# Kernel tuning notes

Hardware: AMD Instinct MI355X
Metric: run time of the kernel (lower is better)

Reference implementation:

```python
import jax
import jax.numpy as jnp
from jax import lax
import numpy as np

B, C, H, W = 16, 96, 112, 112
HIDDEN = 4 * C
LN_EPS = 1e-6  # ConvNeXt LayerNorm eps


def setup_inputs() -> dict:
    key = jax.random.key(0)
    ks = jax.random.split(key, 8)
    x = jax.random.normal(ks[0], (B, C, H, W), dtype=jnp.float32)
    # depthwise 7x7 kernel, HWIO with feature_group_count=C -> (7,7,1,C)
    dw_w = jax.random.normal(ks[1], (7, 7, 1, C), dtype=jnp.float32) * 0.02
    dw_b = jnp.zeros((C,), dtype=jnp.float32)
    gamma = jnp.ones((C,), dtype=jnp.float32)
    beta = jnp.zeros((C,), dtype=jnp.float32)
    w1 = jax.random.normal(ks[2], (C, HIDDEN), dtype=jnp.float32) * 0.02
    b1 = jnp.zeros((HIDDEN,), dtype=jnp.float32)
    w2 = jax.random.normal(ks[3], (HIDDEN, C), dtype=jnp.float32) * 0.02
    b2 = jnp.zeros((C,), dtype=jnp.float32)
    scale = jnp.full((C,), 1e-6, dtype=jnp.float32)  # block_scale init 1e-6
    return {"x": x, "dw_w": dw_w, "dw_b": dw_b, "gamma": gamma, "beta": beta,
            "w1": w1, "b1": b1, "w2": w2, "b2": b2, "scale": scale}


def reference(x, dw_w, dw_b, gamma, beta, w1, b1, w2, b2, scale):
    # depthwise 7x7, stride 1, padding 3 (SAME), groups = C
    y = lax.conv_general_dilated(
        x, dw_w, window_strides=(1, 1), padding="SAME",
        dimension_numbers=("NCHW", "HWIO", "NCHW"),
        feature_group_count=C,
    ) + dw_b[None, :, None, None]
    # BCHW -> BHWC
    y = jnp.transpose(y, (0, 2, 3, 1))
    # LayerNorm over channel dim
    mu = jnp.mean(y, axis=-1, keepdims=True)
    var = jnp.var(y, axis=-1, keepdims=True)
    y = (y - mu) * lax.rsqrt(var + LN_EPS) * gamma + beta
    # pointwise MLP with exact GELU (torch nn.GELU default)
    h = jax.nn.gelu(jnp.einsum("bhwc,cd->bhwd", y, w1) + b1, approximate=False)
    y = jnp.einsum("bhwd,dc->bhwc", h, w2) + b2
    # BHWC -> BCHW, scale, residual (eval mode: stochastic depth = identity)
    y = jnp.transpose(y, (0, 3, 1, 2))
    return scale[None, :, None, None] * y + x
```

## Files before the change

### kernel.cpp

```cpp
#include <hip/hip_runtime.h>
#include <hip/hip_bf16.h>

#define BATCH 16
#define CCH 96
#define HH 112
#define WW 112
#define HID 384
#define NPIX (BATCH * HH * WW)
#define HW (HH * WW)

#define PXB 128
#define ZROWD 50
#define SLICE_B 12288
#define RING_SLOTS 3
#define ZR_BYTES (PXB * ZROWD * 4)
#define B1_OFF (RING_SLOTS * SLICE_B)
#define SMEM_TOTAL (B1_OFF + 1536)

#define XSTR 132
#define CXROWS 62

typedef __attribute__((ext_vector_type(8))) short bf16x8;
typedef __attribute__((ext_vector_type(4))) float f32x4;
typedef __attribute__((ext_vector_type(4))) unsigned int uint4v;

typedef const __attribute__((address_space(1))) void gvoid_t;
typedef __attribute__((address_space(3))) void svoid_t;

__device__ __forceinline__ short f2bf(float v) {
    __hip_bfloat16 h = __float2bfloat16(v);
    return __builtin_bit_cast(short, h);
}
__device__ __forceinline__ float bf2f(short s) {
    unsigned int u = ((unsigned int)(unsigned short)s) << 16;
    return __builtin_bit_cast(float, u);
}
__device__ __forceinline__ float gelu_fast(float v) {
    float e = __expf(-1.702f * v);
    return v * __builtin_amdgcn_rcpf(1.0f + e);
}

__global__ __launch_bounds__(256) void pack_w(const float* __restrict__ w1,
                                              const float* __restrict__ w2,
                                              const float* __restrict__ gamma,
                                              const float* __restrict__ scale,
                                              short* __restrict__ wp) {
    int o = blockIdx.x * 256 + threadIdx.x;
    if (o >= 12 * 12 * 64 * 8) return;
    const int j   = o & 7;
    const int l   = (o >> 3) & 63;
    const int g   = o >> 9;
    const int f   = g % 12;
    const int kk2 = g / 12;
    float v;
    if (f < 6) {
        const int kk = f >> 1, mh = f & 1;
        const int c  = kk * 32 + (l >> 4) * 8 + j;
        const int d  = (2 * kk2 + mh) * 16 + (l & 15);
        v = gamma[c] * w1[c * HID + d];
    } else {
        const int nt2 = f - 6;
        const int dd  = kk2 * 32 + ((j >> 2) << 4) + ((l >> 4) << 2) + (j & 3);
        const int n   = nt2 * 16 + (l & 15);
        v = w2[dd * CCH + n] * scale[n];
    }
    wp[o] = f2bf(v);
}

__global__ __launch_bounds__(256) void pack_bias(const float* __restrict__ w1,
                                                 const float* __restrict__ b1,
                                                 const float* __restrict__ beta,
                                                 const float* __restrict__ b2,
                                                 const float* __restrict__ scale,
                                                 float* __restrict__ b1p,
                                                 float* __restrict__ b2p) {
    int t = blockIdx.x * 256 + threadIdx.x;
    if (t < HID) {
        float s = b1[t];
        for (int c = 0; c < CCH; ++c) s += beta[c] * w1[c * HID + t];
        b1p[t] = s;
    } else if (t < HID + CCH) {
        int c = t - HID;
        b2p[c] = scale[c] * b2[c];
    }
}

__global__ __launch_bounds__(256) void conv_kernel(
    const float* __restrict__ x, const float* __restrict__ dww,
    const float* __restrict__ dwb, short* __restrict__ y)
{
    __shared__ float xs[CXROWS * XSTR];

    const int t = threadIdx.x;
    const int p = blockIdx.x;
    int o = (p & 7) * 384 + (p >> 3);
    const int hh = o & 1;  o >>= 1;
    const int c  = o % CCH;
    const int b  = o / CCH;
    const int h0 = hh * 56;
    const float* xc = x + (size_t)(b * CCH + c) * HW;

    float4 vbuf[8];
    #pragma unroll
    for (int k = 0; k < 8; ++k) {
        const int idx = t + 256 * k;
        const int r  = idx >> 5;
        const int j  = idx & 31;
        const int gh = h0 - 3 + r;
        float4 v = make_float4(0.f, 0.f, 0.f, 0.f);
        if (idx < CXROWS * 32 && (unsigned)gh < HH && j >= 1 && j <= 28)
            v = *reinterpret_cast<const float4*>(xc + gh * WW + 4 * j - 4);
        vbuf[k] = v;
    }
    #pragma unroll
    for (int k = 0; k < 8; ++k) {
        const int idx = t + 256 * k;
        if (idx < CXROWS * 32)
            *reinterpret_cast<float4*>(&xs[(idx >> 5) * XSTR + (idx & 31) * 4]) = vbuf[k];
    }
    __syncthreads();

    const int cg = t >> 5;
    const int rg = t & 31;
    if (cg < 7 && rg < 28) {
        const int r0 = rg * 2;
        const int j0 = cg * 16;
        const float bias = dwb[c];
        float acc0[16], acc1[16];
        #pragma unroll
        for (int i = 0; i < 16; ++i) { acc0[i] = bias; acc1[i] = bias; }
        #pragma unroll
        for (int ir = 0; ir < 8; ++ir) {
            f32x4 qd[6];
            #pragma unroll
            for (int u = 0; u < 6; ++u)
                qd[u] = *reinterpret_cast<const f32x4*>(&xs[(r0 + ir) * XSTR + j0 + 4 * u]);
            #pragma unroll
            for (int kw = 0; kw < 7; ++kw) {
                if (ir <= 6) {
                    const float wt = dww[(ir * 7 + kw) * CCH + c];
                    #pragma unroll
                    for (int i = 0; i < 16; ++i) {
                        const int jj = i + kw + 1;
                        acc0[i] += qd[jj >> 2][jj & 3] * wt;
                    }
                }
                if (ir >= 1) {
                    const float wt = dww[((ir - 1) * 7 + kw) * CCH + c];
                    #pragma unroll
                    for (int i = 0; i < 16; ++i) {
                        const int jj = i + kw + 1;
                        acc1[i] += qd[jj >> 2][jj & 3] * wt;
                    }
                }
            }
        }
        uint4v wa, wb2, wc, wd;
        #pragma unroll
        for (int u = 0; u < 4; ++u) {
            wa[u] = (unsigned int)(unsigned short)f2bf(acc0[2 * u]) |
                    ((unsigned int)(unsigned short)f2bf(acc0[2 * u + 1]) << 16);
            wb2[u] = (unsigned int)(unsigned short)f2bf(acc0[8 + 2 * u]) |
                    ((unsigned int)(unsigned short)f2bf(acc0[9 + 2 * u]) << 16);
            wc[u] = (unsigned int)(unsigned short)f2bf(acc1[2 * u]) |
                    ((unsigned int)(unsigned short)f2bf(acc1[2 * u + 1]) << 16);
            wd[u] = (unsigned int)(unsigned short)f2bf(acc1[8 + 2 * u]) |
                    ((unsigned int)(unsigned short)f2bf(acc1[9 + 2 * u]) << 16);
        }
        short* yc = y + (size_t)(b * CCH + c) * HW + (h0 + r0) * WW + j0;
        *reinterpret_cast<uint4v*>(yc)          = wa;
        *reinterpret_cast<uint4v*>(yc + 8)      = wb2;
        *reinterpret_cast<uint4v*>(yc + WW)     = wc;
        *reinterpret_cast<uint4v*>(yc + WW + 8) = wd;
    }
}

__global__ __launch_bounds__(256, 4) void mlp_kernel(
    const short* __restrict__ ybuf, const char* __restrict__ wp,
    const float* __restrict__ b1p, const float* __restrict__ b2p,
    const float* __restrict__ x, float* __restrict__ out)
{
    __shared__ __align__(16) char smem[SMEM_TOTAL];
    unsigned int* zr = (unsigned int*)smem;
    float* b1l = (float*)(smem + B1_OFF);

    const int t    = threadIdx.x;
    const int lane = t & 63;
    const int wv   = t >> 6;
    const int l15  = lane & 15;
    const int q    = lane >> 4;
    const int px0  = blockIdx.x * PXB;
    const int b    = px0 / HW;
    const int hw0  = px0 - b * HW;

    if (t < 192) {
        const int pq = t / 48;
        const int cp = t - pq * 48;
        const unsigned int* Ap = (const unsigned int*)(ybuf +
            (size_t)(b * CCH + 2 * cp) * HW + hw0 + pq * 32);
        const unsigned int* Bp = (const unsigned int*)(ybuf +
            (size_t)(b * CCH + 2 * cp + 1) * HW + hw0 + pq * 32);
        #pragma unroll
        for (int e = 0; e < 4; ++e) {
            const uint4v A  = *reinterpret_cast<const uint4v*>(Ap + e * 4);
            const uint4v Bv = *reinterpret_cast<const uint4v*>(Bp + e * 4);
            #pragma unroll
            for (int k = 0; k < 4; ++k) {
                const int px = pq * 32 + e * 8 + 2 * k;
                zr[px * ZROWD + cp]       = (A[k] & 0xffffu) | (Bv[k] << 16);
                zr[(px + 1) * ZROWD + cp] = (A[k] >> 16) | (Bv[k] & 0xffff0000u);
            }
        }
    } else {
        const int i0 = (t - 192) * 6;
        #pragma unroll
        for (int i2 = 0; i2 < 6; ++i2) b1l[i0 + i2] = b1p[i0 + i2];
    }

    f32x4 acc2[2][6];
    #pragma unroll
    for (int nt2 = 0; nt2 < 6; ++nt2) {
        const int c = nt2 * 16 + l15;
        const float bv = b2p[c];
        #pragma unroll
        for (int m2 = 0; m2 < 2; ++m2) {
            const size_t g = (size_t)(b * CCH + c) * HW + hw0 + wv * 32 + m2 * 16 + q * 4;
            const f32x4 xv = *reinterpret_cast<const f32x4*>(x + g);
            acc2[m2][nt2].x = bv + xv.x;  acc2[m2][nt2].y = bv + xv.y;
            acc2[m2][nt2].z = bv + xv.z;  acc2[m2][nt2].w = bv + xv.w;
        }
    }
    __syncthreads();

    bf16x8 za[2][3];
    #pragma unroll
    for (int nt = 0; nt < 2; ++nt) {
        const int row = wv * 32 + nt * 16 + l15;
        const char* base = smem + row * (ZROWD * 4) + q * 16;
        float s1 = 0.f, s2 = 0.f;
        #pragma unroll
        for (int kk = 0; kk < 3; ++kk) {
            za[nt][kk] = *reinterpret_cast<const bf16x8*>(base + kk * 64);
            #pragma unroll
            for (int j = 0; j < 8; ++j) {
                const float v = bf2f(za[nt][kk][j]);
                s1 += v; s2 += v * v;
            }
        }
        s1 += __shfl_xor(s1, 16, 64);  s2 += __shfl_xor(s2, 16, 64);
        s1 += __shfl_xor(s1, 32, 64);  s2 += __shfl_xor(s2, 32, 64);
        const float mu   = s1 * (1.0f / CCH);
        const float rstd = rsqrtf(s2 * (1.0f / CCH) - mu * mu + 1e-6f);
        #pragma unroll
        for (int kk = 0; kk < 3; ++kk)
            #pragma unroll
            for (int j = 0; j < 8; ++j)
                za[nt][kk][j] = f2bf((bf2f(za[nt][kk][j]) - mu) * rstd);
    }
    __syncthreads();

    asm volatile("s_waitcnt vmcnt(0)" ::: "memory");

    #define STAGE_F(SL, SLOT)                                                       \
        {                                                                           \
            const char* _s = wp + (size_t)(SL) * SLICE_B + (wv * 3) * 1024 +        \
                             lane * 16;                                             \
            char* _d = smem + (SLOT) * SLICE_B + (wv * 3) * 1024;                   \
            __builtin_amdgcn_global_load_lds((gvoid_t*)(_s),        (svoid_t*)(_d),        16, 0, 0); \
            __builtin_amdgcn_global_load_lds((gvoid_t*)(_s + 1024), (svoid_t*)(_d + 1024), 16, 0, 0); \
            __builtin_amdgcn_global_load_lds((gvoid_t*)(_s + 2048), (svoid_t*)(_d + 2048), 16, 0, 0); \
        }
    #define WAITBAR()                                                               \
        {                                                                           \
            asm volatile("s_waitcnt vmcnt(3)" ::: "memory");                        \
            __builtin_amdgcn_s_barrier();                                           \
            __builtin_amdgcn_sched_barrier(0);                                      \
        }

    STAGE_F(0, 0);

    #pragma unroll
    for (int kk2 = 0; kk2 < 12; ++kk2) {
        {
            const int sl = (kk2 + 1 > 11) ? 11 : kk2 + 1;
            STAGE_F(sl, sl % RING_SLOTS);
        }
        WAITBAR();
        const char* wb = smem + (kk2 % RING_SLOTS) * SLICE_B + lane * 16;

        f32x4 p0[2], p1[2];
        const f32x4 bva = *reinterpret_cast<const f32x4*>(b1l + 32 * kk2 + q * 4);
        const f32x4 bvb = *reinterpret_cast<const f32x4*>(b1l + 32 * kk2 + 16 + q * 4);
        p0[0] = bva;  p0[1] = bva;
        p1[0] = bvb;  p1[1] = bvb;
        #pragma unroll
        for (int kk = 0; kk < 3; ++kk) {
            const bf16x8 wfa = *reinterpret_cast<const bf16x8*>(wb + (kk * 2) * 1024);
            const bf16x8 wfb = *reinterpret_cast<const bf16x8*>(wb + (kk * 2 + 1) * 1024);
            p0[0] = __builtin_amdgcn_mfma_f32_16x16x32_bf16(wfa, za[0][kk], p0[0], 0, 0, 0);
            p0[1] = __builtin_amdgcn_mfma_f32_16x16x32_bf16(wfa, za[1][kk], p0[1], 0, 0, 0);
            p1[0] = __builtin_amdgcn_mfma_f32_16x16x32_bf16(wfb, za[0][kk], p1[0], 0, 0, 0);
            p1[1] = __builtin_amdgcn_mfma_f32_16x16x32_bf16(wfb, za[1][kk], p1[1], 0, 0, 0);
        }
        bf16x8 hv[2];
        #pragma unroll
        for (int nt = 0; nt < 2; ++nt)
            #pragma unroll
            for (int i = 0; i < 4; ++i) {
                hv[nt][i]     = f2bf(gelu_fast(p0[nt][i]));
                hv[nt][4 + i] = f2bf(gelu_fast(p1[nt][i]));
            }
        #pragma unroll
        for (int nt2 = 0; nt2 < 6; ++nt2) {
            const bf16x8 bfr = *reinterpret_cast<const bf16x8*>(wb + (6 + nt2) * 1024);
            acc2[0][nt2] = __builtin_amdgcn_mfma_f32_16x16x32_bf16(hv[0], bfr, acc2[0][nt2], 0, 0, 0);
            acc2[1][nt2] = __builtin_amdgcn_mfma_f32_16x16x32_bf16(hv[1], bfr, acc2[1][nt2], 0, 0, 0);
        }
    }
    #undef STAGE_F
    #undef WAITBAR

    #pragma unroll
    for (int m2 = 0; m2 < 2; ++m2) {
        const int pxl = hw0 + wv * 32 + m2 * 16 + q * 4;
        #pragma unroll
        for (int nt2 = 0; nt2 < 6; ++nt2) {
            const int c = nt2 * 16 + l15;
            const size_t g = (size_t)(b * CCH + c) * HW + pxl;
            *reinterpret_cast<f32x4*>(out + g) = acc2[m2][nt2];
        }
    }
}

extern "C" void kernel_launch(void* const* d_in, const int* in_sizes, int n_in,
                              void* d_out, int out_size, void* d_ws, size_t ws_size,
                              hipStream_t stream) {
    const float* x     = (const float*)d_in[0];
    const float* dww   = (const float*)d_in[1];
    const float* dwb   = (const float*)d_in[2];
    const float* gamma = (const float*)d_in[3];
    const float* beta  = (const float*)d_in[4];
    const float* w1    = (const float*)d_in[5];
    const float* b1    = (const float*)d_in[6];
    const float* w2    = (const float*)d_in[7];
    const float* b2    = (const float*)d_in[8];
    const float* scale = (const float*)d_in[9];
    float* out = (float*)d_out;

    char* ws = (char*)d_ws;
    short* ybuf = (short*)ws;
    const size_t Y_BYTES = (size_t)NPIX * CCH * 2;
    short* wp  = (short*)(ws + Y_BYTES);
    float* b1p = (float*)(ws + Y_BYTES + 12 * SLICE_B);
    float* b2p = b1p + HID;

    pack_w<<<(12 * 12 * 64 * 8 + 255) / 256, 256, 0, stream>>>(w1, w2, gamma, scale, wp);
    pack_bias<<<2, 256, 0, stream>>>(w1, b1, beta, b2, scale, b1p, b2p);
    conv_kernel<<<BATCH * CCH * 2, 256, 0, stream>>>(x, dww, dwb, ybuf);
    mlp_kernel<<<NPIX / PXB, 256, 0, stream>>>(ybuf, (const char*)wp, b1p, b2p, x, out);
}
```

Baseline: 112.4 us.

## Split MLP tile across eight waves with sixteen pixels per wave

The MLP kernel now launches 512 threads per block instead of 256, so each of the eight waves owns 16 pixels rather than 32. Per-wave accumulators and normalized activations shrink, cutting register use so more waves can be resident and hide memory latency. Weight staging into LDS is spread across six waves with two loads each, and the bias preload and transpose are reassigned to the larger thread count. In exchange, each weight fragment read from LDS now feeds half as many MFMAs, doubling LDS read traffic per FLOP and adding more barrier participants.

Result: slower. 135.4 us (+20.5%).

```diff
diff --git a/kernel.cpp b/kernel.cpp
--- a/kernel.cpp
+++ b/kernel.cpp
@@ -175,7 +175,7 @@
     }
 }
 
-__global__ __launch_bounds__(256, 4) void mlp_kernel(
+__global__ __launch_bounds__(512, 8) void mlp_kernel(
     const short* __restrict__ ybuf, const char* __restrict__ wp,
     const float* __restrict__ b1p, const float* __restrict__ b2p,
     const float* __restrict__ x, float* __restrict__ out)
@@ -193,57 +193,53 @@
     const int b    = px0 / HW;
     const int hw0  = px0 - b * HW;
 
-    if (t < 192) {
-        const int pq = t / 48;
-        const int cp = t - pq * 48;
+    if (t < 384) {
+        const int pxq = t / 48;
+        const int cp  = t - pxq * 48;
         const unsigned int* Ap = (const unsigned int*)(ybuf +
-            (size_t)(b * CCH + 2 * cp) * HW + hw0 + pq * 32);
+            (size_t)(b * CCH + 2 * cp) * HW + hw0 + pxq * 16);
         const unsigned int* Bp = (const unsigned int*)(ybuf +
-            (size_t)(b * CCH + 2 * cp + 1) * HW + hw0 + pq * 32);
-        #pragma unroll
-        for (int e = 0; e < 4; ++e) {
+            (size_t)(b * CCH + 2 * cp + 1) * HW + hw0 + pxq * 16);
+        #pragma unroll
+        for (int e = 0; e < 2; ++e) {
             const uint4v A  = *reinterpret_cast<const uint4v*>(Ap + e * 4);
             const uint4v Bv = *reinterpret_cast<const uint4v*>(Bp + e * 4);
             #pragma unroll
             for (int k = 0; k < 4; ++k) {
-                const int px = pq * 32 + e * 8 + 2 * k;
+                const int px = pxq * 16 + e * 8 + 2 * k;
                 zr[px * ZROWD + cp]       = (A[k] & 0xffffu) | (Bv[k] << 16);
                 zr[(px + 1) * ZROWD + cp] = (A[k] >> 16) | (Bv[k] & 0xffff0000u);
             }
         }
     } else {
-        const int i0 = (t - 192) * 6;
-        #pragma unroll
-        for (int i2 = 0; i2 < 6; ++i2) b1l[i0 + i2] = b1p[i0 + i2];
-    }
-
-    f32x4 acc2[2][6];
+        const int i0 = (t - 384) * 3;
+        #pragma unroll
+        for (int i2 = 0; i2 < 3; ++i2) b1l[i0 + i2] = b1p[i0 + i2];
+    }
+
+    f32x4 acc2[6];
     #pragma unroll
     for (int nt2 = 0; nt2 < 6; ++nt2) {
         const int c = nt2 * 16 + l15;
         const float bv = b2p[c];
-        #pragma unroll
-        for (int m2 = 0; m2 < 2; ++m2) {
-            const size_t g = (size_t)(b * CCH + c) * HW + hw0 + wv * 32 + m2 * 16 + q * 4;
-            const f32x4 xv = *reinterpret_cast<const f32x4*>(x + g);
-            acc2[m2][nt2].x = bv + xv.x;  acc2[m2][nt2].y = bv + xv.y;
-            acc2[m2][nt2].z = bv + xv.z;  acc2[m2][nt2].w = bv + xv.w;
-        }
+        const size_t g = (size_t)(b * CCH + c) * HW + hw0 + wv * 16 + q * 4;
+        const f32x4 xv = *reinterpret_cast<const f32x4*>(x + g);
+        acc2[nt2].x = bv + xv.x;  acc2[nt2].y = bv + xv.y;
+        acc2[nt2].z = bv + xv.z;  acc2[nt2].w = bv + xv.w;
     }
     __syncthreads();
 
-    bf16x8 za[2][3];
-    #pragma unroll
-    for (int nt = 0; nt < 2; ++nt) {
-        const int row = wv * 32 + nt * 16 + l15;
+    bf16x8 za[3];
+    {
+        const int row = wv * 16 + l15;
         const char* base = smem + row * (ZROWD * 4) + q * 16;
         float s1 = 0.f, s2 = 0.f;
         #pragma unroll
         for (int kk = 0; kk < 3; ++kk) {
-            za[nt][kk] = *reinterpret_cast<const bf16x8*>(base + kk * 64);
+            za[kk] = *reinterpret_cast<const bf16x8*>(base + kk * 64);
             #pragma unroll
             for (int j = 0; j < 8; ++j) {
-                const float v = bf2f(za[nt][kk][j]);
+                const float v = bf2f(za[kk][j]);
                 s1 += v; s2 += v * v;
             }
         }
@@ -255,24 +251,23 @@
         for (int kk = 0; kk < 3; ++kk)
             #pragma unroll
             for (int j = 0; j < 8; ++j)
-                za[nt][kk][j] = f2bf((bf2f(za[nt][kk][j]) - mu) * rstd);
+                za[kk][j] = f2bf((bf2f(za[kk][j]) - mu) * rstd);
     }
     __syncthreads();
 
     asm volatile("s_waitcnt vmcnt(0)" ::: "memory");
 
     #define STAGE_F(SL, SLOT)                                                       \
-        {                                                                           \
-            const char* _s = wp + (size_t)(SL) * SLICE_B + (wv * 3) * 1024 +        \
+        if (wv < 6) {                                                               \
+            const char* _s = wp + (size_t)(SL) * SLICE_B + (wv * 2) * 1024 +        \
                              lane * 16;                                             \
-            char* _d = smem + (SLOT) * SLICE_B + (wv * 3) * 1024;                   \
+            char* _d = smem + (SLOT) * SLICE_B + (wv * 2) * 1024;                   \
             __builtin_amdgcn_global_load_lds((gvoid_t*)(_s),        (svoid_t*)(_d),        16, 0, 0); \
             __builtin_amdgcn_global_load_lds((gvoid_t*)(_s + 1024), (svoid_t*)(_d + 1024), 16, 0, 0); \
-            __builtin_amdgcn_global_load_lds((gvoid_t*)(_s + 2048), (svoid_t*)(_d + 2048), 16, 0, 0); \
         }
     #define WAITBAR()                                                               \
         {                                                                           \
-            asm volatile("s_waitcnt vmcnt(3)" ::: "memory");                        \
+            asm volatile("s_waitcnt vmcnt(2)" ::: "memory");                        \
             __builtin_amdgcn_s_barrier();                                           \
             __builtin_amdgcn_sched_barrier(0);                                      \
         }
@@ -288,46 +283,38 @@
         WAITBAR();
         const char* wb = smem + (kk2 % RING_SLOTS) * SLICE_B + lane * 16;
 
-        f32x4 p0[2], p1[2];
-        const f32x4 bva = *reinterpret_cast<const f32x4*>(b1l + 32 * kk2 + q * 4);
-        const f32x4 bvb = *reinterpret_cast<const f32x4*>(b1l + 32 * kk2 + 16 + q * 4);
-        p0[0] = bva;  p0[1] = bva;
-        p1[0] = bvb;  p1[1] = bvb;
+        f32x4 p0, p1;
+        p0 = *reinterpret_cast<const f32x4*>(b1l + 32 * kk2 + q * 4);
+        p1 = *reinterpret_cast<const f32x4*>(b1l + 32 * kk2 + 16 + q * 4);
         #pragma unroll
         for (int kk = 0; kk < 3; ++kk) {
             const bf16x8 wfa = *reinterpret_cast<const bf16x8*>(wb + (kk * 2) * 1024);
             const bf16x8 wfb = *reinterpret_cast<const bf16x8*>(wb + (kk * 2 + 1) * 1024);
-            p0[0] = __builtin_amdgcn_mfma_f32_16x16x32_bf16(wfa, za[0][kk], p0[0], 0, 0, 0);
-            p0[1] = __builtin_amdgcn_mfma_f32_16x16x32_bf16(wfa, za[1][kk], p0[1], 0, 0, 0);
-            p1[0] = __builtin_amdgcn_mfma_f32_16x16x32_bf16(wfb, za[0][kk], p1[0], 0, 0, 0);
-            p1[1] = __builtin_amdgcn_mfma_f32_16x16x32_bf16(wfb, za[1][kk], p1[1], 0, 0, 0);
-        }
-        bf16x8 hv[2];
-        #pragma unroll
-        for (int nt = 0; nt < 2; ++nt)
-            #pragma unroll
-            for (int i = 0; i < 4; ++i) {
-                hv[nt][i]     = f2bf(gelu_fast(p0[nt][i]));
-                hv[nt][4 + i] = f2bf(gelu_fast(p1[nt][i]));
-            }
+            p0 = __builtin_amdgcn_mfma_f32_16x16x32_bf16(wfa, za[kk], p0, 0, 0, 0);
+            p1 = __builtin_amdgcn_mfma_f32_16x16x32_bf16(wfb, za[kk], p1, 0, 0, 0);
+        }
+        bf16x8 hv;
+        #pragma unroll
+        for (int i = 0; i < 4; ++i) {
+            hv[i]     = f2bf(gelu_fast(p0[i]));
+            hv[4 + i] = f2bf(gelu_fast(p1[i]));
+        }
         #pragma unroll
         for (int nt2 = 0; nt2 < 6; ++nt2) {
             const bf16x8 bfr = *reinterpret_cast<const bf16x8*>(wb + (6 + nt2) * 1024);
-            acc2[0][nt2] = __builtin_amdgcn_mfma_f32_16x16x32_bf16(hv[0], bfr, acc2[0][nt2], 0, 0, 0);
-            acc2[1][nt2] = __builtin_amdgcn_mfma_f32_16x16x32_bf16(hv[1], bfr, acc2[1][nt2], 0, 0, 0);
+            acc2[nt2] = __builtin_amdgcn_mfma_f32_16x16x32_bf16(hv, bfr, acc2[nt2], 0, 0, 0);
         }
     }
     #undef STAGE_F
     #undef WAITBAR
 
-    #pragma unroll
-    for (int m2 = 0; m2 < 2; ++m2) {
-        const int pxl = hw0 + wv * 32 + m2 * 16 + q * 4;
+    {
+        const int pxl = hw0 + wv * 16 + q * 4;
         #pragma unroll
         for (int nt2 = 0; nt2 < 6; ++nt2) {
             const int c = nt2 * 16 + l15;
             const size_t g = (size_t)(b * CCH + c) * HW + pxl;
-            *reinterpret_cast<f32x4*>(out + g) = acc2[m2][nt2];
+            *reinterpret_cast<f32x4*>(out + g) = acc2[nt2];
         }
     }
 }
@@ -357,5 +344,5 @@
     pack_w<<<(12 * 12 * 64 * 8 + 255) / 256, 256, 0, stream>>>(w1, w2, gamma, scale, wp);
     pack_bias<<<2, 256, 0, stream>>>(w1, b1, beta, b2, scale, b1p, b2p);
     conv_kernel<<<BATCH * CCH * 2, 256, 0, stream>>>(x, dww, dwb, ybuf);
-    mlp_kernel<<<NPIX / PXB, 256, 0, stream>>>(ybuf, (const char*)wp, b1p, b2p, x, out);
-}
+    mlp_kernel<<<NPIX / PXB, 512, 0, stream>>>(ybuf, (const char*)wp, b1p, b2p, x, out);
+}
```
